# Kernel optimization log

Hardware: AMD Instinct MI355X
Metric: run time of the kernel (lower is better)

## Reference

```python
import jax, jax.numpy as jnp
import numpy as np

T_STEPS = 64  # fixed number of greedy decode steps (original loops until EOS)


def setup_inputs() -> dict:
    key = jax.random.key(0)
    ks = jax.random.split(key, 10)
    E, H, Z, V = 512, 1024, 64, 50257
    s = 0.05
    return {
        "z": jax.random.normal(ks[0], (1, Z), jnp.float32),
        "eos_embed": jax.random.normal(ks[1], (E,), jnp.float32) * 0.1,
        "W_ih": jax.random.normal(ks[2], (3 * H, E), jnp.float32) * s,
        "W_hh": jax.random.normal(ks[3], (3 * H, H), jnp.float32) * s,
        "b_ih": jax.random.normal(ks[4], (3 * H,), jnp.float32) * s,
        "b_hh": jax.random.normal(ks[5], (3 * H,), jnp.float32) * s,
        "W_dec": jax.random.normal(ks[6], (Z, H), jnp.float32) * s,
        "b_dec": jax.random.normal(ks[7], (H,), jnp.float32) * s,
        "W_vocab": jax.random.normal(ks[8], (H, V), jnp.float32) * s,
        "b_vocab": jax.random.normal(ks[9], (V,), jnp.float32) * s,
    }


def reference(z, eos_embed, W_ih, W_hh, b_ih, b_hh, W_dec, b_dec, W_vocab, b_vocab):
    H = W_hh.shape[1]
    # hidden = self.decode(z) -> initial GRU hidden state, [H]
    h0 = (z @ W_dec + b_dec)[0]
    # input to every step is the constant EOS embedding; precompute input gates
    gi = W_ih @ eos_embed + b_ih                     # [3H]
    gi_r, gi_z, gi_n = gi[:H], gi[H:2 * H], gi[2 * H:]

    def step(h, _):
        gh = W_hh @ h + b_hh                          # [3H]
        gh_r, gh_z, gh_n = gh[:H], gh[H:2 * H], gh[2 * H:]
        r = jax.nn.sigmoid(gi_r + gh_r)
        u = jax.nn.sigmoid(gi_z + gh_z)
        n = jnp.tanh(gi_n + r * gh_n)
        h_new = (1.0 - u) * n + u * h
        logits = h_new @ W_vocab + b_vocab            # [V]
        log_p = jax.nn.log_softmax(logits)
        tok = jnp.argmax(log_p).astype(jnp.int32)
        return h_new, (log_p, tok)

    _, (log_p, seq) = jax.lax.scan(step, h0, None, length=T_STEPS)
    return log_p, seq  # [T, V] float, [T] int32
```

## Files before the change

### kernel.cpp

```cpp
#include <hip/hip_runtime.h>

#define HD   1024
#define G3   3072
#define ED   512
#define ZD   64
#define VV   50257
#define TT   64
#define BT   512

#define OFF_HINIT 0
#define OFF_HALL  1024
#define OFF_HALLT 66560
#define OFF_GI    132096
#define OFF_PMAX  135168
#define OFF_PIDX  135424
#define OFF_PSUM  135680

__global__ __launch_bounds__(BT) void k_init(
    const float* __restrict__ z,    const float* __restrict__ eos,
    const float* __restrict__ Wih,  const float* __restrict__ bih,
    const float* __restrict__ Wdec, const float* __restrict__ bdec,
    float* __restrict__ ws)
{
    const int tid = threadIdx.x;
    const int b   = blockIdx.x;
    float* h_init = ws + OFF_HINIT;
    float* gi     = ws + OFF_GI;

    if (b == 384) {
        #pragma unroll
        for (int rep = 0; rep < 2; ++rep) {
            int j = tid + rep * BT;
            float acc = bdec[j];
            #pragma unroll
            for (int i = 0; i < ZD; ++i)
                acc = fmaf(z[i], Wdec[i * HD + j], acc);
            h_init[j] = acc;
        }
    } else {
        const int gtid = b * BT + tid;
        const int w    = gtid >> 6;
        const int lane = tid & 63;
        const float* wp = Wih + (size_t)w * ED + lane;
        float d = 0.f;
        #pragma unroll
        for (int i = 0; i < 8; ++i) d = fmaf(wp[i * 64], eos[lane + i * 64], d);
        #pragma unroll
        for (int off = 32; off; off >>= 1) d += __shfl_xor(d, off, 64);
        if (lane == 0) gi[w] = d + bih[w];
    }
}

__global__ __launch_bounds__(BT) void k_step(
    const float* __restrict__ Whh, const float* __restrict__ bhh,
    float* __restrict__ ws, int t)
{
    const int tid  = threadIdx.x;
    const int gtid = blockIdx.x * BT + tid;
    const int w    = gtid >> 6;
    const int lane = tid & 63;

    float* h_init = ws + OFF_HINIT;
    float* h_all  = ws + OFF_HALL;
    float* h_allT = ws + OFF_HALLT;
    const float* gi = ws + OFF_GI;

    const float* hp = (t == 0) ? h_init : (h_all + (size_t)(t - 1) * HD);
    const float* r0 = Whh + (size_t)w * HD + lane;
    const float* r1 = Whh + (size_t)(w + HD) * HD + lane;
    const float* r2 = Whh + (size_t)(w + 2 * HD) * HD + lane;

    float d0 = 0.f, d1 = 0.f, d2 = 0.f;
    #pragma unroll
    for (int i = 0; i < 16; ++i) {
        float hv = hp[lane + i * 64];
        d0 = fmaf(r0[i * 64], hv, d0);
        d1 = fmaf(r1[i * 64], hv, d1);
        d2 = fmaf(r2[i * 64], hv, d2);
    }
    #pragma unroll
    for (int off = 32; off; off >>= 1) {
        d0 += __shfl_xor(d0, off, 64);
        d1 += __shfl_xor(d1, off, 64);
        d2 += __shfl_xor(d2, off, 64);
    }
    if (lane == 0) {
        float ghr = d0 + bhh[w];
        float ghz = d1 + bhh[w + HD];
        float ghn = d2 + bhh[w + 2 * HD];
        float r = 1.f / (1.f + expf(-(gi[w] + ghr)));
        float u = 1.f / (1.f + expf(-(gi[w + HD] + ghz)));
        float n = tanhf(gi[w + 2 * HD] + r * ghn);
        float hn = (1.f - u) * n + u * hp[w];
        h_all[(size_t)t * HD + w]  = hn;
        h_allT[(size_t)w * TT + t] = hn;
    }
}

#define FMA4(ACC, S) do { ACC.x = fmaf(w4.x,(S),ACC.x); ACC.y = fmaf(w4.y,(S),ACC.y); \
                          ACC.z = fmaf(w4.z,(S),ACC.z); ACC.w = fmaf(w4.w,(S),ACC.w); } while(0)

__global__ __launch_bounds__(BT) void k_gemm(
    const float* __restrict__ Wv, const float* __restrict__ bv,
    const float* __restrict__ hT,
    float* __restrict__ out)
{
    const int tid = threadIdx.x;
    const int kp  = tid & 3;
    const int vgl = (tid >> 2) & 15;
    const int tq  = tid >> 6;
    const int t0  = tq << 3;
    const int vg  = blockIdx.x * 16 + vgl;
    const int v0  = vg << 2;
    const bool fullv = (v0 + 3 < VV);
    const bool vx = (v0 < VV);

    __shared__ __align__(16) float sh_hS[2][4368];

    float4 acc[8];
    #pragma unroll
    for (int i = 0; i < 8; ++i) acc[i] = make_float4(0.f, 0.f, 0.f, 0.f);

    float* shS = &sh_hS[0][0];
    auto stage = [&](int c, int bufsel) {
        float4* dst = (float4*)(shS + bufsel * 4368);
        const float4* src = (const float4*)hT;
        #pragma unroll
        for (int jj = 0; jj < 2; ++jj) {
            int f4 = jj * BT + tid;
            int t4 = f4 & 15;
            int rest = f4 >> 4;
            int kk = rest & 15, kps = rest >> 4;
            int k = kps * 256 + c * 16 + kk;
            dst[kps * 273 + kk * 17 + t4] = src[k * 16 + t4];
        }
    };
    stage(0, 0);

    for (int c = 0; c < 16; ++c) {
        __syncthreads();
        if (c < 15) stage(c + 1, (c + 1) & 1);
        const float* shbuf = shS + (c & 1) * 4368 + kp * 1092 + t0;
        const float* wrow = Wv + (size_t)(kp * 256 + c * 16) * VV + v0;
        #pragma unroll
        for (int kk = 0; kk < 16; ++kk) {
            const float* wp = wrow + (size_t)kk * VV;
            float4 w4;
            if (fullv) { w4.x = wp[0]; w4.y = wp[1]; w4.z = wp[2]; w4.w = wp[3]; }
            else { w4.x = vx ? wp[0] : 0.f; w4.y = 0.f; w4.z = 0.f; w4.w = 0.f; }
            const float* sf = shbuf + kk * 68;
            float4 ha = ((const float4*)sf)[0];
            float4 hb = ((const float4*)sf)[1];
            FMA4(acc[0], ha.x); FMA4(acc[1], ha.y); FMA4(acc[2], ha.z); FMA4(acc[3], ha.w);
            FMA4(acc[4], hb.x); FMA4(acc[5], hb.y); FMA4(acc[6], hb.z); FMA4(acc[7], hb.w);
        }
    }

    #pragma unroll
    for (int i = 0; i < 8; ++i) {
        float4 a = acc[i];
        a.x += __shfl_xor(a.x, 1, 64); a.y += __shfl_xor(a.y, 1, 64);
        a.z += __shfl_xor(a.z, 1, 64); a.w += __shfl_xor(a.w, 1, 64);
        a.x += __shfl_xor(a.x, 2, 64); a.y += __shfl_xor(a.y, 2, 64);
        a.z += __shfl_xor(a.z, 2, 64); a.w += __shfl_xor(a.w, 2, 64);
        acc[i] = a;
    }

    if (kp == 0) {
        float bx = 0.f, by = 0.f, bz = 0.f, bw = 0.f;
        if (fullv) { bx = bv[v0]; by = bv[v0 + 1]; bz = bv[v0 + 2]; bw = bv[v0 + 3]; }
        else if (vx) bx = bv[v0];
        #pragma unroll
        for (int tt = 0; tt < 8; ++tt) {
            float4 a = acc[tt];
            float* op = out + (size_t)(t0 + tt) * VV + v0;
            if (fullv) { op[0] = a.x + bx; op[1] = a.y + by; op[2] = a.z + bz; op[3] = a.w + bw; }
            else if (vx) { op[0] = a.x + bx; }
        }
    }
}

#define RSB 512
#define QCH 12576
__global__ __launch_bounds__(RSB) void k_rowstat(
    const float* __restrict__ out,
    float* __restrict__ pMax, int* __restrict__ pIdx, float* __restrict__ pSum)
{
    const int t   = blockIdx.x >> 2;
    const int q   = blockIdx.x & 3;
    const int tid = threadIdx.x;
    const int start = q * QCH;
    const int end   = (start + QCH < VV) ? (start + QCH) : VV;
    const float* row = out + (size_t)t * VV;

    __shared__ float sm[RSB];
    __shared__ int   si[RSB];

    float m = -3.4e38f; int mi = start;
    for (int i = start + tid; i < end; i += RSB) {
        float v = row[i];
        if (v > m) { m = v; mi = i; }
    }
    sm[tid] = m; si[tid] = mi;
    __syncthreads();
    for (int s = RSB / 2; s; s >>= 1) {
        if (tid < s) {
            float om = sm[tid + s]; int oi = si[tid + s];
            if (om > sm[tid] || (om == sm[tid] && oi < si[tid])) { sm[tid] = om; si[tid] = oi; }
        }
        __syncthreads();
    }
    const float M = sm[0];
    const int   I = si[0];
    __syncthreads();

    float s = 0.f;
    for (int i = start + tid; i < end; i += RSB) s += expf(row[i] - M);
    sm[tid] = s;
    __syncthreads();
    for (int st = RSB / 2; st; st >>= 1) {
        if (tid < st) sm[tid] += sm[tid + st];
        __syncthreads();
    }
    if (tid == 0) { pMax[blockIdx.x] = M; pIdx[blockIdx.x] = I; pSum[blockIdx.x] = sm[0]; }
}

__global__ __launch_bounds__(BT) void k_final(
    const float* __restrict__ pMax, const int* __restrict__ pIdx,
    const float* __restrict__ pSum, float* __restrict__ out)
{
    __shared__ float s_lz[TT];
    const int tid  = threadIdx.x;
    const int gtid = blockIdx.x * BT + tid;
    if (tid < TT) {
        float M = -3.4e38f; int I = 0;
        #pragma unroll
        for (int q = 0; q < 4; ++q) {
            float m = pMax[tid * 4 + q];
            if (m > M) { M = m; I = pIdx[tid * 4 + q]; }
        }
        float S = 0.f;
        #pragma unroll
        for (int q = 0; q < 4; ++q)
            S += pSum[tid * 4 + q] * expf(pMax[tid * 4 + q] - M);
        s_lz[tid] = M + logf(S);
        if (blockIdx.x == 0) out[(size_t)TT * VV + tid] = (float)I;
    }
    __syncthreads();

    const int total  = TT * VV;
    const int stride = 393 * BT;
    #pragma unroll
    for (int r = 0; r < 16; ++r) {
        int idx = gtid + r * stride;
        if (idx < total) {
            int t = idx / VV;
            out[idx] = out[idx] - s_lz[t];
        }
    }
}

extern "C" void kernel_launch(void* const* d_in, const int* in_sizes, int n_in,
                              void* d_out, int out_size, void* d_ws, size_t ws_size,
                              hipStream_t stream) {
    (void)in_sizes; (void)n_in; (void)out_size; (void)ws_size;
    const float* z    = (const float*)d_in[0];
    const float* eos  = (const float*)d_in[1];
    const float* Wih  = (const float*)d_in[2];
    const float* Whh  = (const float*)d_in[3];
    const float* bih  = (const float*)d_in[4];
    const float* bhh  = (const float*)d_in[5];
    const float* Wdec = (const float*)d_in[6];
    const float* bdec = (const float*)d_in[7];
    const float* Wv   = (const float*)d_in[8];
    const float* bv   = (const float*)d_in[9];
    float* out = (float*)d_out;
    float* ws  = (float*)d_ws;

    hipLaunchKernelGGL(k_init, dim3(385), dim3(BT), 0, stream,
                       z, eos, Wih, bih, Wdec, bdec, ws);
    for (int t = 0; t < TT; ++t)
        hipLaunchKernelGGL(k_step, dim3(128), dim3(BT), 0, stream, Whh, bhh, ws, t);
    hipLaunchKernelGGL(k_gemm, dim3(786), dim3(BT), 0, stream,
                       Wv, bv, ws + OFF_HALLT, out);
    hipLaunchKernelGGL(k_rowstat, dim3(256), dim3(RSB), 0, stream,
                       out, ws + OFF_PMAX, (int*)(ws + OFF_PIDX), ws + OFF_PSUM);
    hipLaunchKernelGGL(k_final, dim3(393), dim3(BT), 0, stream,
                       ws + OFF_PMAX, (const int*)(ws + OFF_PIDX), ws + OFF_PSUM, out);
}
```

Before: 841.9 us.

## Fuse GRU steps into one persistent kernel with grid barrier, simplify GEMM

The 64 per-step GRU launches become a single persistent kernel of 128 blocks. Blocks synchronise between steps with an atomic-counter grid barrier, and the recurrent weight rows are read with float4 loads. The vocab GEMM no longer stages h in LDS with double buffering and reads it straight from global memory through the cache. This removes launch overhead on the serial recurrence, but relies on all blocks being co-resident and could make the GEMM's h reads less efficient.

Result: slower. 3.271 ms (+288.6%).

```diff
diff --git a/kernel.cpp b/kernel.cpp
--- a/kernel.cpp
+++ b/kernel.cpp
@@ -7,6 +7,7 @@
 #define VV   50257
 #define TT   64
 #define BT   512
+#define NBS  128
 
 #define OFF_HINIT 0
 #define OFF_HALL  1024
@@ -15,6 +16,7 @@
 #define OFF_PMAX  135168
 #define OFF_PIDX  135424
 #define OFF_PSUM  135680
+#define OFF_CNT   135936
 
 __global__ __launch_bounds__(BT) void k_init(
     const float* __restrict__ z,    const float* __restrict__ eos,
@@ -26,6 +28,8 @@
     const int b   = blockIdx.x;
     float* h_init = ws + OFF_HINIT;
     float* gi     = ws + OFF_GI;
+
+    if (b == 0 && tid == 0) *(unsigned int*)(ws + OFF_CNT) = 0u;
 
     if (b == 384) {
         #pragma unroll
@@ -51,49 +55,70 @@
     }
 }
 
-__global__ __launch_bounds__(BT) void k_step(
+__global__ __launch_bounds__(BT) void k_steps(
     const float* __restrict__ Whh, const float* __restrict__ bhh,
-    float* __restrict__ ws, int t)
+    float* __restrict__ ws)
 {
     const int tid  = threadIdx.x;
-    const int gtid = blockIdx.x * BT + tid;
-    const int w    = gtid >> 6;
     const int lane = tid & 63;
+    const int w    = blockIdx.x * 8 + (tid >> 6);
 
     float* h_init = ws + OFF_HINIT;
     float* h_all  = ws + OFF_HALL;
     float* h_allT = ws + OFF_HALLT;
     const float* gi = ws + OFF_GI;
-
-    const float* hp = (t == 0) ? h_init : (h_all + (size_t)(t - 1) * HD);
-    const float* r0 = Whh + (size_t)w * HD + lane;
-    const float* r1 = Whh + (size_t)(w + HD) * HD + lane;
-    const float* r2 = Whh + (size_t)(w + 2 * HD) * HD + lane;
-
-    float d0 = 0.f, d1 = 0.f, d2 = 0.f;
-    #pragma unroll
-    for (int i = 0; i < 16; ++i) {
-        float hv = hp[lane + i * 64];
-        d0 = fmaf(r0[i * 64], hv, d0);
-        d1 = fmaf(r1[i * 64], hv, d1);
-        d2 = fmaf(r2[i * 64], hv, d2);
-    }
-    #pragma unroll
-    for (int off = 32; off; off >>= 1) {
-        d0 += __shfl_xor(d0, off, 64);
-        d1 += __shfl_xor(d1, off, 64);
-        d2 += __shfl_xor(d2, off, 64);
-    }
-    if (lane == 0) {
-        float ghr = d0 + bhh[w];
-        float ghz = d1 + bhh[w + HD];
-        float ghn = d2 + bhh[w + 2 * HD];
-        float r = 1.f / (1.f + expf(-(gi[w] + ghr)));
-        float u = 1.f / (1.f + expf(-(gi[w + HD] + ghz)));
-        float n = tanhf(gi[w + 2 * HD] + r * ghn);
-        float hn = (1.f - u) * n + u * hp[w];
-        h_all[(size_t)t * HD + w]  = hn;
-        h_allT[(size_t)w * TT + t] = hn;
+    unsigned int* cnt = (unsigned int*)(ws + OFF_CNT);
+
+    const float4* W4  = (const float4*)Whh;
+    const float4* r0p = W4 + (size_t)w * 256 + lane * 4;
+    const float4* r1p = W4 + (size_t)(w + HD) * 256 + lane * 4;
+    const float4* r2p = W4 + (size_t)(w + 2 * HD) * 256 + lane * 4;
+
+    const float g0 = gi[w], g1 = gi[w + HD], g2 = gi[w + 2 * HD];
+    const float b0 = bhh[w], b1 = bhh[w + HD], b2 = bhh[w + 2 * HD];
+
+    for (int t = 0; t < TT; ++t) {
+        const float* hp   = (t == 0) ? h_init : (h_all + (size_t)(t - 1) * HD);
+        const float4* hp4 = (const float4*)hp + lane * 4;
+
+        float d0 = 0.f, d1 = 0.f, d2 = 0.f;
+        #pragma unroll
+        for (int j = 0; j < 4; ++j) {
+            float4 hv = hp4[j];
+            float4 a0 = r0p[j];
+            float4 a1 = r1p[j];
+            float4 a2 = r2p[j];
+            d0 = fmaf(a0.x, hv.x, d0); d0 = fmaf(a0.y, hv.y, d0);
+            d0 = fmaf(a0.z, hv.z, d0); d0 = fmaf(a0.w, hv.w, d0);
+            d1 = fmaf(a1.x, hv.x, d1); d1 = fmaf(a1.y, hv.y, d1);
+            d1 = fmaf(a1.z, hv.z, d1); d1 = fmaf(a1.w, hv.w, d1);
+            d2 = fmaf(a2.x, hv.x, d2); d2 = fmaf(a2.y, hv.y, d2);
+            d2 = fmaf(a2.z, hv.z, d2); d2 = fmaf(a2.w, hv.w, d2);
+        }
+        #pragma unroll
+        for (int off = 32; off; off >>= 1) {
+            d0 += __shfl_xor(d0, off, 64);
+            d1 += __shfl_xor(d1, off, 64);
+            d2 += __shfl_xor(d2, off, 64);
+        }
+        if (lane == 0) {
+            float r = 1.f / (1.f + expf(-(g0 + d0 + b0)));
+            float u = 1.f / (1.f + expf(-(g1 + d1 + b1)));
+            float n = tanhf(g2 + r * (d2 + b2));
+            float hn = (1.f - u) * n + u * hp[w];
+            h_all[(size_t)t * HD + w]  = hn;
+            h_allT[(size_t)w * TT + t] = hn;
+        }
+        __threadfence();
+        __syncthreads();
+        if (tid == 0) {
+            atomicAdd(cnt, 1u);
+            while (__hip_atomic_load(cnt, __ATOMIC_ACQUIRE, __HIP_MEMORY_SCOPE_AGENT)
+                   < (unsigned int)(NBS * (t + 1)))
+                __builtin_amdgcn_s_sleep(1);
+        }
+        __syncthreads();
+        __threadfence();
     }
 }
 
@@ -115,45 +140,24 @@
     const bool fullv = (v0 + 3 < VV);
     const bool vx = (v0 < VV);
 
-    __shared__ __align__(16) float sh_hS[2][4368];
-
     float4 acc[8];
     #pragma unroll
     for (int i = 0; i < 8; ++i) acc[i] = make_float4(0.f, 0.f, 0.f, 0.f);
 
-    float* shS = &sh_hS[0][0];
-    auto stage = [&](int c, int bufsel) {
-        float4* dst = (float4*)(shS + bufsel * 4368);
-        const float4* src = (const float4*)hT;
-        #pragma unroll
-        for (int jj = 0; jj < 2; ++jj) {
-            int f4 = jj * BT + tid;
-            int t4 = f4 & 15;
-            int rest = f4 >> 4;
-            int kk = rest & 15, kps = rest >> 4;
-            int k = kps * 256 + c * 16 + kk;
-            dst[kps * 273 + kk * 17 + t4] = src[k * 16 + t4];
-        }
-    };
-    stage(0, 0);
-
-    for (int c = 0; c < 16; ++c) {
-        __syncthreads();
-        if (c < 15) stage(c + 1, (c + 1) & 1);
-        const float* shbuf = shS + (c & 1) * 4368 + kp * 1092 + t0;
-        const float* wrow = Wv + (size_t)(kp * 256 + c * 16) * VV + v0;
-        #pragma unroll
-        for (int kk = 0; kk < 16; ++kk) {
-            const float* wp = wrow + (size_t)kk * VV;
-            float4 w4;
-            if (fullv) { w4.x = wp[0]; w4.y = wp[1]; w4.z = wp[2]; w4.w = wp[3]; }
-            else { w4.x = vx ? wp[0] : 0.f; w4.y = 0.f; w4.z = 0.f; w4.w = 0.f; }
-            const float* sf = shbuf + kk * 68;
-            float4 ha = ((const float4*)sf)[0];
-            float4 hb = ((const float4*)sf)[1];
-            FMA4(acc[0], ha.x); FMA4(acc[1], ha.y); FMA4(acc[2], ha.z); FMA4(acc[3], ha.w);
-            FMA4(acc[4], hb.x); FMA4(acc[5], hb.y); FMA4(acc[6], hb.z); FMA4(acc[7], hb.w);
-        }
+    const float4* hTb = (const float4*)hT + (t0 >> 2);
+    const int kbase = kp * 256;
+
+    #pragma unroll 4
+    for (int kk = 0; kk < 256; ++kk) {
+        const int k = kbase + kk;
+        const float* wp = Wv + (size_t)k * VV + v0;
+        float4 w4;
+        if (fullv) { w4.x = wp[0]; w4.y = wp[1]; w4.z = wp[2]; w4.w = wp[3]; }
+        else { w4.x = vx ? wp[0] : 0.f; w4.y = 0.f; w4.z = 0.f; w4.w = 0.f; }
+        float4 ha = hTb[k * 16];
+        float4 hb = hTb[k * 16 + 1];
+        FMA4(acc[0], ha.x); FMA4(acc[1], ha.y); FMA4(acc[2], ha.z); FMA4(acc[3], ha.w);
+        FMA4(acc[4], hb.x); FMA4(acc[5], hb.y); FMA4(acc[6], hb.z); FMA4(acc[7], hb.w);
     }
 
     #pragma unroll
@@ -279,8 +283,7 @@
 
     hipLaunchKernelGGL(k_init, dim3(385), dim3(BT), 0, stream,
                        z, eos, Wih, bih, Wdec, bdec, ws);
-    for (int t = 0; t < TT; ++t)
-        hipLaunchKernelGGL(k_step, dim3(128), dim3(BT), 0, stream, Whh, bhh, ws, t);
+    hipLaunchKernelGGL(k_steps, dim3(NBS), dim3(BT), 0, stream, Whh, bhh, ws);
     hipLaunchKernelGGL(k_gemm, dim3(786), dim3(BT), 0, stream,
                        Wv, bv, ws + OFF_HALLT, out);
     hipLaunchKernelGGL(k_rowstat, dim3(256), dim3(RSB), 0, stream,
```
